# Performance work log

Hardware: AMD Instinct MI355X
Metric: run time of the kernel (lower is better)

## Reference

```python
import jax, jax.numpy as jnp
import numpy as np

H = 4          # attention heads
C = 64         # per-head channels (hidden_size)
NEG_SLOPE = 0.2  # PyG GATConv default negative_slope


def _gat_layer(x, W, a_src, a_dst, b, src, dst):
    """PyG-style GATConv (concat=True) on one graph. x: [N, F]."""
    N = x.shape[0]
    h = (x @ W).reshape(N, H, C)                      # [N, H, C]
    s_src = jnp.sum(h * a_src, axis=-1)               # [N, H]
    s_dst = jnp.sum(h * a_dst, axis=-1)               # [N, H]
    e = jax.nn.leaky_relu(s_src[src] + s_dst[dst], NEG_SLOPE)   # [E, H]
    # softmax over incoming edges of each destination node
    m = jax.ops.segment_max(e, dst, num_segments=N)   # [N, H]
    m = jnp.where(jnp.isfinite(m), m, 0.0)
    ex = jnp.exp(e - m[dst])
    denom = jax.ops.segment_sum(ex, dst, num_segments=N)
    alpha = ex / denom[dst]                           # [E, H]
    out = jax.ops.segment_sum(h[src] * alpha[:, :, None], dst, num_segments=N)
    return out.reshape(N, H * C) + b                  # [N, H*C]


def setup_inputs() -> dict:
    key = jax.random.key(0)
    ks = jax.random.split(key, 12)
    B, N, F = 2, 20000, 128
    E = 320000
    HC = H * C  # 256
    x = jax.random.normal(ks[0], (B, N, F), dtype=jnp.float32)
    edge_index = jax.random.randint(ks[1], (2, E), 0, N, dtype=jnp.int64)
    def glorot(k, shape):
        fan = shape[0] + shape[-1]
        return jax.random.normal(k, shape, dtype=jnp.float32) * np.sqrt(2.0 / fan)
    return {
        "x": x,
        "edge_index": edge_index,
        "W1": glorot(ks[2], (F, HC)),
        "a_src1": glorot(ks[3], (H, C)),
        "a_dst1": glorot(ks[4], (H, C)),
        "b1": jnp.zeros((HC,), jnp.float32),
        "W2": glorot(ks[5], (HC, HC)),
        "a_src2": glorot(ks[6], (H, C)),
        "a_dst2": glorot(ks[7], (H, C)),
        "b2": jnp.zeros((HC,), jnp.float32),
        "Wf": glorot(ks[8], (HC, C)),
        "bf": jnp.zeros((C,), jnp.float32),
    }


def reference(x, edge_index, W1, a_src1, a_dst1, b1, W2, a_src2, a_dst2, b2, Wf, bf):
    B, N, _ = x.shape
    sl = jnp.arange(N, dtype=edge_index.dtype)        # self loops (PyG default)
    src = jnp.concatenate([edge_index[0], sl])
    dst = jnp.concatenate([edge_index[1], sl])
    h = jax.vmap(lambda xi: _gat_layer(xi, W1, a_src1, a_dst1, b1, src, dst))(x)
    h = jax.nn.elu(h)
    h = jax.vmap(lambda xi: _gat_layer(xi, W2, a_src2, a_dst2, b2, src, dst))(h)
    return h @ Wf + bf                                 # [B, N, hidden]
```

## Files before the change

kernel.cpp:

```cpp
#include <hip/hip_runtime.h>
#include <math.h>

#define NN 20000
#define NE 320000
#define ETOT (NE + NN)
#define NH 4
#define CH 64
#define HC 256
#define FIN 128
#define NEG_SLOPE 0.2f
#define CAP 64
#define EST 68
#define AGG_TPB 128

typedef unsigned short ushort_t;
typedef unsigned int uint_t;
typedef _Float16 half8 __attribute__((ext_vector_type(8)));
typedef float f32x4 __attribute__((ext_vector_type(4)));

__device__ __forceinline__ ushort_t f2h_bits(float f) {
    union { _Float16 h; ushort_t u; } c; c.h = (_Float16)f;
    return c.u;
}


__global__ void k_zero_i32(int* __restrict__ p, int n) {
    int i = blockIdx.x * blockDim.x + threadIdx.x;
    if (i < n) p[i] = 0;
}

__global__ void k_hist(const int* __restrict__ ei, int* __restrict__ counts) {
    int e = blockIdx.x * blockDim.x + threadIdx.x;
    if (e >= ETOT) return;
    int d = (e < NE) ? ei[NE + e] : (e - NE);
    atomicAdd(&counts[d], 1);
}

__global__ void k_scan(const int* __restrict__ counts, int* __restrict__ rowptr,
                       int* __restrict__ cursor) {
    __shared__ int part[1024];
    int tid = threadIdx.x;
    const int n = NN;
    int chunk = (n + 1023) / 1024;
    int b = tid * chunk;
    int e = min(b + chunk, n);
    int s = 0;
    for (int i = b; i < e; ++i) s += counts[i];
    part[tid] = s;
    __syncthreads();
    for (int off = 1; off < 1024; off <<= 1) {
        int v = (tid >= off) ? part[tid - off] : 0;
        __syncthreads();
        part[tid] += v;
        __syncthreads();
    }
    int ex = (tid > 0) ? part[tid - 1] : 0;
    for (int i = b; i < e; ++i) { rowptr[i] = ex; cursor[i] = ex; ex += counts[i]; }
    if (tid == 1023) rowptr[n] = part[1023];
}

__global__ void k_scatter(const int* __restrict__ ei, int* __restrict__ cursor,
                          int* __restrict__ col) {
    int e = blockIdx.x * blockDim.x + threadIdx.x;
    if (e >= ETOT) return;
    int s, d;
    if (e < NE) { s = ei[e]; d = ei[NE + e]; }
    else        { s = e - NE; d = s; }
    int pos = atomicAdd(&cursor[d], 1);
    col[pos] = s;
}


#define SN1 (FIN * HC)
#define SN2 (SN1 + HC * HC)
#define SN3 (SN2 + HC * CH)
#define SN4 (SN3 + (2 * NN * FIN) / 4)

__global__ void k_setup(const float* __restrict__ x, const float* __restrict__ W1,
                        const float* __restrict__ W2, const float* __restrict__ Wf,
                        ushort_t* __restrict__ Xh, ushort_t* __restrict__ Wt1,
                        ushort_t* __restrict__ Wt2, ushort_t* __restrict__ Wtf) {
    int i = blockIdx.x * blockDim.x + threadIdx.x;
    if (i < SN1) {
        int n = i / FIN, k = i - n * FIN;
        Wt1[i] = f2h_bits(W1[(size_t)k * HC + n]);
    } else if (i < SN2) {
        int j = i - SN1;
        int n = j / HC, k = j - n * HC;
        Wt2[j] = f2h_bits(W2[(size_t)k * HC + n]);
    } else if (i < SN3) {
        int j = i - SN2;
        int n = j / HC, k = j - n * HC;
        Wtf[j] = f2h_bits(Wf[(size_t)k * CH + n]);
    } else if (i < SN4) {
        int j = (i - SN3) * 4;
        float4 v = *reinterpret_cast<const float4*>(&x[j]);
        ushort4 u;
        u.x = f2h_bits(v.x); u.y = f2h_bits(v.y); u.z = f2h_bits(v.z); u.w = f2h_bits(v.w);
        *reinterpret_cast<ushort4*>(&Xh[j]) = u;
    }
}


__global__ __launch_bounds__(256) void k_gemm128(const ushort_t* __restrict__ A,
                                                 const ushort_t* __restrict__ Bt,
                                                 ushort_t* __restrict__ Ch,
                                                 const float* __restrict__ a_src,
                                                 const float* __restrict__ a_dst,
                                                 float* __restrict__ ssrc,
                                                 float* __restrict__ sdst,
                                                 int M, int K, int NC) {
    __shared__ ushort_t As[128 * 40];
    __shared__ ushort_t Bs[128 * 40];
    int tid = threadIdx.x;
    int wave = tid >> 6, lane = tid & 63;
    int wr = wave >> 1, wc = wave & 1;
    int row0 = blockIdx.x * 128, col0 = blockIdx.y * 128;

    f32x4 acc[4][4];
#pragma unroll
    for (int i = 0; i < 4; ++i)
#pragma unroll
        for (int j = 0; j < 4; ++j) acc[i][j] = (f32x4){0.f, 0.f, 0.f, 0.f};

    int srow = tid >> 2;
    int sk8 = (tid & 3) * 8;
    int l15 = lane & 15, lk = (lane >> 4) * 8;

    int ra0 = min(row0 + srow, M - 1);
    int ra1 = min(row0 + 64 + srow, M - 1);

    for (int k0 = 0; k0 < K; k0 += 32) {
        uint4 a0 = *reinterpret_cast<const uint4*>(&A[(size_t)ra0 * K + k0 + sk8]);
        uint4 a1 = *reinterpret_cast<const uint4*>(&A[(size_t)ra1 * K + k0 + sk8]);
        uint4 b0 = *reinterpret_cast<const uint4*>(&Bt[(size_t)(col0 + srow) * K + k0 + sk8]);
        uint4 b1 = *reinterpret_cast<const uint4*>(&Bt[(size_t)(col0 + 64 + srow) * K + k0 + sk8]);
        __syncthreads();
        *reinterpret_cast<uint4*>(&As[srow * 40 + sk8]) = a0;
        *reinterpret_cast<uint4*>(&As[(64 + srow) * 40 + sk8]) = a1;
        *reinterpret_cast<uint4*>(&Bs[srow * 40 + sk8]) = b0;
        *reinterpret_cast<uint4*>(&Bs[(64 + srow) * 40 + sk8]) = b1;
        __syncthreads();

        half8 af[4], bf_[4];
#pragma unroll
        for (int m = 0; m < 4; ++m)
            af[m] = *reinterpret_cast<const half8*>(&As[(wr * 64 + m * 16 + l15) * 40 + lk]);
#pragma unroll
        for (int nf = 0; nf < 4; ++nf)
            bf_[nf] = *reinterpret_cast<const half8*>(&Bs[(wc * 64 + nf * 16 + l15) * 40 + lk]);
#pragma unroll
        for (int m = 0; m < 4; ++m)
#pragma unroll
            for (int nf = 0; nf < 4; ++nf)
                acc[m][nf] = __builtin_amdgcn_mfma_f32_16x16x32_f16(af[m], bf_[nf], acc[m][nf], 0, 0, 0);
    }

#pragma unroll
    for (int m = 0; m < 4; ++m)
#pragma unroll
        for (int nf = 0; nf < 4; ++nf) {
            int colc = col0 + wc * 64 + nf * 16 + l15;
#pragma unroll
            for (int j = 0; j < 4; ++j) {
                int row = row0 + wr * 64 + m * 16 + (lane >> 4) * 4 + j;
                if (row < M) Ch[(size_t)row * NC + colc] = f2h_bits(acc[m][nf][j]);
            }
        }

    if (ssrc) {
        int head = (col0 >> 6) + wc;
        float as4[4], ad4[4];
#pragma unroll
        for (int nf = 0; nf < 4; ++nf) {
            as4[nf] = a_src[head * 64 + nf * 16 + l15];
            ad4[nf] = a_dst[head * 64 + nf * 16 + l15];
        }
#pragma unroll
        for (int m = 0; m < 4; ++m)
#pragma unroll
            for (int j = 0; j < 4; ++j) {
                float ps = acc[m][0][j] * as4[0] + acc[m][1][j] * as4[1]
                         + acc[m][2][j] * as4[2] + acc[m][3][j] * as4[3];
                float pd = acc[m][0][j] * ad4[0] + acc[m][1][j] * ad4[1]
                         + acc[m][2][j] * ad4[2] + acc[m][3][j] * ad4[3];
#pragma unroll
                for (int off = 1; off < 16; off <<= 1) {
                    ps += __shfl_xor(ps, off);
                    pd += __shfl_xor(pd, off);
                }
                int row = row0 + wr * 64 + m * 16 + (lane >> 4) * 4 + j;
                if (l15 == 0 && row < M) {
                    ssrc[(size_t)row * NH + head] = ps;
                    sdst[(size_t)row * NH + head] = pd;
                }
            }
    }
}


__global__ __launch_bounds__(256) void k_gemm_mfma(const ushort_t* __restrict__ A,
                                                   const ushort_t* __restrict__ Bt,
                                                   float* __restrict__ Cf,
                                                   const float* __restrict__ bias,
                                                   int M, int K, int NC) {
    __shared__ ushort_t As[64][40];
    __shared__ ushort_t Bs[64][40];
    int tid = threadIdx.x;
    int wave = tid >> 6, lane = tid & 63;
    int wr = wave >> 1, wc = wave & 1;
    int row0 = blockIdx.x * 64, col0 = blockIdx.y * 64;

    f32x4 acc[2][2];
#pragma unroll
    for (int i = 0; i < 2; ++i)
#pragma unroll
        for (int j = 0; j < 2; ++j) acc[i][j] = (f32x4){0.f, 0.f, 0.f, 0.f};

    int sr = tid >> 2;
    int sk = (tid & 3) * 8;
    int l15 = lane & 15, lk = (lane >> 4) * 8;

    for (int k0 = 0; k0 < K; k0 += 32) {
        uint4 av = make_uint4(0, 0, 0, 0);
        int rowg = row0 + sr;
        if (rowg < M) av = *reinterpret_cast<const uint4*>(&A[(size_t)rowg * K + k0 + sk]);
        uint4 bv = *reinterpret_cast<const uint4*>(&Bt[(size_t)(col0 + sr) * K + k0 + sk]);
        __syncthreads();
        *reinterpret_cast<uint4*>(&As[sr][sk]) = av;
        *reinterpret_cast<uint4*>(&Bs[sr][sk]) = bv;
        __syncthreads();

        half8 a0 = *reinterpret_cast<const half8*>(&As[wr * 32 + l15][lk]);
        half8 a1 = *reinterpret_cast<const half8*>(&As[wr * 32 + 16 + l15][lk]);
        half8 b0 = *reinterpret_cast<const half8*>(&Bs[wc * 32 + l15][lk]);
        half8 b1 = *reinterpret_cast<const half8*>(&Bs[wc * 32 + 16 + l15][lk]);
        acc[0][0] = __builtin_amdgcn_mfma_f32_16x16x32_f16(a0, b0, acc[0][0], 0, 0, 0);
        acc[0][1] = __builtin_amdgcn_mfma_f32_16x16x32_f16(a0, b1, acc[0][1], 0, 0, 0);
        acc[1][0] = __builtin_amdgcn_mfma_f32_16x16x32_f16(a1, b0, acc[1][0], 0, 0, 0);
        acc[1][1] = __builtin_amdgcn_mfma_f32_16x16x32_f16(a1, b1, acc[1][1], 0, 0, 0);
    }

#pragma unroll
    for (int fr = 0; fr < 2; ++fr)
#pragma unroll
        for (int fc = 0; fc < 2; ++fc) {
            int colc = col0 + wc * 32 + fc * 16 + l15;
#pragma unroll
            for (int j = 0; j < 4; ++j) {
                int row = row0 + wr * 32 + fr * 16 + (lane >> 4) * 4 + j;
                if (row < M) Cf[(size_t)row * NC + colc] = acc[fr][fc][j] + bias[colc];
            }
        }
}


__global__ __launch_bounds__(AGG_TPB) void k_agg(const ushort_t* __restrict__ hb,
                                                 const float* __restrict__ ssrc,
                                                 const float* __restrict__ sdst,
                                                 const int* __restrict__ rowptr,
                                                 const int* __restrict__ col,
                                                 const float* __restrict__ bias,
                                                 ushort_t* __restrict__ outh,
                                                 int do_elu) {
    __shared__ int cols_lds[AGG_TPB / 64][CAP];
    __shared__ float e_lds[AGG_TPB / 64][4 * EST];
    int wave = threadIdx.x >> 6, lane = threadIdx.x & 63;
    int gw = blockIdx.x * (AGG_TPB / 64) + wave;
    int b = (gw >= NN) ? 1 : 0;
    int n = gw - b * NN;
    int* colw = cols_lds[wave];
    float* ew = e_lds[wave];
    int start = rowptr[n];
    int deg = rowptr[n + 1] - start;
    int es = lane >> 5;
    int cg = lane & 31;
    int hd = cg >> 3;

    const ushort_t* hbase = hb + (size_t)b * NN * HC;
    const float* ssrcb = ssrc + (size_t)b * NN * NH;

    float sd[4];
    {
        float4 s0 = *reinterpret_cast<const float4*>(&sdst[((size_t)b * NN + n) * NH]);
        sd[0] = s0.x; sd[1] = s0.y; sd[2] = s0.z; sd[3] = s0.w;
    }

    float pd[4], acc[8];
#pragma unroll
    for (int c = 0; c < 4; ++c) pd[c] = 0.f;
#pragma unroll
    for (int j = 0; j < 8; ++j) acc[j] = 0.f;

    const int cg8 = cg * 8;

    for (int c0 = 0; c0 < deg; c0 += CAP) {
        int cnt = min(CAP, deg - c0);
        int cnt4 = (cnt + 3) & ~3;

        for (int i = lane; i < cnt4; i += 64) {
            if (i < cnt) {
                int s = col[start + c0 + i];
                colw[i] = s * HC;
                float4 p = *reinterpret_cast<const float4*>(&ssrcb[(size_t)s * NH]);
                float e[4];
                e[0] = p.x + sd[0]; e[1] = p.y + sd[1]; e[2] = p.z + sd[2]; e[3] = p.w + sd[3];
#pragma unroll
                for (int c = 0; c < 4; ++c) {
                    e[c] = fmaxf(e[c], NEG_SLOPE * e[c]);
                    float w = __expf(e[c]);
                    ew[c * EST + i] = w;
                    pd[c] += w;
                }
            } else {
                colw[i] = 0;
#pragma unroll
                for (int c = 0; c < 4; ++c) ew[c * EST + i] = 0.f;
            }
        }

        for (int i = 0; i < cnt4; i += 4) {
            int i0 = i + es, i1 = i + 2 + es;
            int o0 = colw[i0], o1 = colw[i1];
            float w0 = ew[hd * EST + i0], w1 = ew[hd * EST + i1];
            half8 v0 = *reinterpret_cast<const half8*>(hbase + o0 + cg8);
            half8 v1 = *reinterpret_cast<const half8*>(hbase + o1 + cg8);
#pragma unroll
            for (int j = 0; j < 8; ++j) acc[j] = fmaf((float)v0[j], w0, acc[j]);
#pragma unroll
            for (int j = 0; j < 8; ++j) acc[j] = fmaf((float)v1[j], w1, acc[j]);
        }
    }

#pragma unroll
    for (int off = 32; off > 0; off >>= 1)
#pragma unroll
        for (int c = 0; c < 4; ++c) pd[c] += __shfl_xor(pd[c], off);

#pragma unroll
    for (int j = 0; j < 8; ++j) acc[j] += __shfl_xor(acc[j], 32);

    if (es == 0) {
        float inv = 1.0f / pd[hd];
        float4 b0 = *reinterpret_cast<const float4*>(&bias[cg8]);
        float4 b1 = *reinterpret_cast<const float4*>(&bias[cg8 + 4]);
        float bv[8] = {b0.x, b0.y, b0.z, b0.w, b1.x, b1.y, b1.z, b1.w};
        ushort_t o[8];
#pragma unroll
        for (int j = 0; j < 8; ++j) {
            float r = acc[j] * inv + bv[j];
            if (do_elu && r < 0.f) r = expm1f(r);
            o[j] = f2h_bits(r);
        }
        *reinterpret_cast<uint4*>(&outh[((size_t)b * NN + n) * HC + cg8]) =
            *reinterpret_cast<uint4*>(&o[0]);
    }
}


extern "C" void kernel_launch(void* const* d_in, const int* in_sizes, int n_in,
                              void* d_out, int out_size, void* d_ws, size_t ws_size,
                              hipStream_t stream) {
    const float* x      = (const float*)d_in[0];
    const int*   ei     = (const int*)d_in[1];
    const float* W1     = (const float*)d_in[2];
    const float* a_src1 = (const float*)d_in[3];
    const float* a_dst1 = (const float*)d_in[4];
    const float* b1     = (const float*)d_in[5];
    const float* W2     = (const float*)d_in[6];
    const float* a_src2 = (const float*)d_in[7];
    const float* a_dst2 = (const float*)d_in[8];
    const float* b2     = (const float*)d_in[9];
    const float* Wf     = (const float*)d_in[10];
    const float* bf     = (const float*)d_in[11];
    float* out = (float*)d_out;

    const int M2 = 2 * NN;
    float* ws = (float*)d_ws;
    float* Ssrc = ws;
    float* Sdst = Ssrc + (size_t)M2 * NH;
    ushort_t* Hb16 = (ushort_t*)(Sdst + (size_t)M2 * NH);
    ushort_t* Ob16 = Hb16 + (size_t)M2 * HC;
    ushort_t* Xb16 = Ob16 + (size_t)M2 * HC;
    ushort_t* Wt1  = Xb16 + (size_t)M2 * FIN;
    ushort_t* Wt2  = Wt1 + (size_t)HC * FIN;
    ushort_t* Wtf  = Wt2 + (size_t)HC * HC;
    int* counts = (int*)(Wtf + (size_t)CH * HC);
    int* rowptr = counts + NN;
    int* cursor = rowptr + (NN + 1);
    int* colidx = cursor + NN;

    k_zero_i32<<<(NN + 255) / 256, 256, 0, stream>>>(counts, NN);
    k_hist<<<(ETOT + 255) / 256, 256, 0, stream>>>(ei, counts);
    k_scan<<<1, 1024, 0, stream>>>(counts, rowptr, cursor);
    k_scatter<<<(ETOT + 255) / 256, 256, 0, stream>>>(ei, cursor, colidx);

    k_setup<<<(SN4 + 255) / 256, 256, 0, stream>>>(x, W1, W2, Wf, Xb16, Wt1, Wt2, Wtf);

    const int gM128 = (M2 + 127) / 128;
    const int gAgg = M2 / (AGG_TPB / 64);
    k_gemm128<<<dim3(gM128, HC / 128), 256, 0, stream>>>(Xb16, Wt1, Hb16, a_src1, a_dst1,
                                                         Ssrc, Sdst, M2, FIN, HC);
    k_agg<<<gAgg, AGG_TPB, 0, stream>>>(Hb16, Ssrc, Sdst, rowptr, colidx, b1, Ob16, 1);
    k_gemm128<<<dim3(gM128, HC / 128), 256, 0, stream>>>(Ob16, Wt2, Hb16, a_src2, a_dst2,
                                                         Ssrc, Sdst, M2, HC, HC);
    k_agg<<<gAgg, AGG_TPB, 0, stream>>>(Hb16, Ssrc, Sdst, rowptr, colidx, b2, Ob16, 0);
    k_gemm_mfma<<<dim3((M2 + 63) / 64, CH / 64), 256, 0, stream>>>(Ob16, Wtf, out, bf, M2, HC, CH);
}
```

Baseline: 221.5 us.

## Parallelize CSR row-pointer scan and make aggregation a persistent grid-stride kernel

```diff
diff --git a/kernel.cpp b/kernel.cpp
--- a/kernel.cpp
+++ b/kernel.cpp
@@ -11,7 +11,9 @@
 #define NEG_SLOPE 0.2f
 #define CAP 64
 #define EST 68
-#define AGG_TPB 128
+#define SCB 79
+#define AGG_BLOCKS 2048
+#define AGG_SLOTS (AGG_BLOCKS * 4)
 
 typedef unsigned short ushort_t;
 typedef unsigned int uint_t;
@@ -36,27 +38,54 @@
     atomicAdd(&counts[d], 1);
 }
 
-__global__ void k_scan(const int* __restrict__ counts, int* __restrict__ rowptr,
-                       int* __restrict__ cursor) {
-    __shared__ int part[1024];
-    int tid = threadIdx.x;
-    const int n = NN;
-    int chunk = (n + 1023) / 1024;
-    int b = tid * chunk;
-    int e = min(b + chunk, n);
-    int s = 0;
-    for (int i = b; i < e; ++i) s += counts[i];
-    part[tid] = s;
+__global__ void k_scan_part(const int* __restrict__ counts, int* __restrict__ bsum) {
+    __shared__ int red[256];
+    int t = threadIdx.x;
+    int i = blockIdx.x * 256 + t;
+    red[t] = (i < NN) ? counts[i] : 0;
     __syncthreads();
-    for (int off = 1; off < 1024; off <<= 1) {
-        int v = (tid >= off) ? part[tid - off] : 0;
-        __syncthreads();
-        part[tid] += v;
-        __syncthreads();
-    }
-    int ex = (tid > 0) ? part[tid - 1] : 0;
-    for (int i = b; i < e; ++i) { rowptr[i] = ex; cursor[i] = ex; ex += counts[i]; }
-    if (tid == 1023) rowptr[n] = part[1023];
+#pragma unroll
+    for (int off = 128; off > 0; off >>= 1) {
+        if (t < off) red[t] += red[t + off];
+        __syncthreads();
+    }
+    if (t == 0) bsum[blockIdx.x] = red[0];
+}
+
+__global__ void k_scan_top(const int* __restrict__ bsum, int* __restrict__ bpre) {
+    __shared__ int s[128];
+    int t = threadIdx.x;
+    int own = (t < SCB) ? bsum[t] : 0;
+    s[t] = own;
+    __syncthreads();
+#pragma unroll
+    for (int off = 1; off < 128; off <<= 1) {
+        int v = (t >= off) ? s[t - off] : 0;
+        __syncthreads();
+        s[t] += v;
+        __syncthreads();
+    }
+    if (t < SCB) bpre[t] = s[t] - own;
+}
+
+__global__ void k_scan_apply(const int* __restrict__ counts, const int* __restrict__ bpre,
+                             int* __restrict__ rowptr, int* __restrict__ cursor) {
+    __shared__ int s[256];
+    int t = threadIdx.x;
+    int i = blockIdx.x * 256 + t;
+    int c = (i < NN) ? counts[i] : 0;
+    s[t] = c;
+    __syncthreads();
+#pragma unroll
+    for (int off = 1; off < 256; off <<= 1) {
+        int v = (t >= off) ? s[t - off] : 0;
+        __syncthreads();
+        s[t] += v;
+        __syncthreads();
+    }
+    int ex = s[t] - c + bpre[blockIdx.x];
+    if (i < NN) { rowptr[i] = ex; cursor[i] = ex; }
+    if (i == NN - 1) rowptr[NN] = ex + c;
 }
 
 __global__ void k_scatter(const int* __restrict__ ei, int* __restrict__ cursor,
@@ -255,105 +284,108 @@
 }
 
 
-__global__ __launch_bounds__(AGG_TPB) void k_agg(const ushort_t* __restrict__ hb,
-                                                 const float* __restrict__ ssrc,
-                                                 const float* __restrict__ sdst,
-                                                 const int* __restrict__ rowptr,
-                                                 const int* __restrict__ col,
-                                                 const float* __restrict__ bias,
-                                                 ushort_t* __restrict__ outh,
-                                                 int do_elu) {
-    __shared__ int cols_lds[AGG_TPB / 64][CAP];
-    __shared__ float e_lds[AGG_TPB / 64][4 * EST];
+__global__ __launch_bounds__(256) void k_agg(const ushort_t* __restrict__ hb,
+                                             const float* __restrict__ ssrc,
+                                             const float* __restrict__ sdst,
+                                             const int* __restrict__ rowptr,
+                                             const int* __restrict__ col,
+                                             const float* __restrict__ bias,
+                                             ushort_t* __restrict__ outh,
+                                             int do_elu) {
+    __shared__ int cols_lds[4][CAP];
+    __shared__ float e_lds[4][4 * EST];
     int wave = threadIdx.x >> 6, lane = threadIdx.x & 63;
-    int gw = blockIdx.x * (AGG_TPB / 64) + wave;
-    int b = (gw >= NN) ? 1 : 0;
-    int n = gw - b * NN;
+    int slot = blockIdx.x * 4 + wave;
     int* colw = cols_lds[wave];
     float* ew = e_lds[wave];
-    int start = rowptr[n];
-    int deg = rowptr[n + 1] - start;
     int es = lane >> 5;
     int cg = lane & 31;
     int hd = cg >> 3;
-
-    const ushort_t* hbase = hb + (size_t)b * NN * HC;
-    const float* ssrcb = ssrc + (size_t)b * NN * NH;
-
-    float sd[4];
-    {
-        float4 s0 = *reinterpret_cast<const float4*>(&sdst[((size_t)b * NN + n) * NH]);
-        sd[0] = s0.x; sd[1] = s0.y; sd[2] = s0.z; sd[3] = s0.w;
-    }
-
-    float pd[4], acc[8];
-#pragma unroll
-    for (int c = 0; c < 4; ++c) pd[c] = 0.f;
-#pragma unroll
-    for (int j = 0; j < 8; ++j) acc[j] = 0.f;
-
     const int cg8 = cg * 8;
 
-    for (int c0 = 0; c0 < deg; c0 += CAP) {
-        int cnt = min(CAP, deg - c0);
-        int cnt4 = (cnt + 3) & ~3;
-
-        for (int i = lane; i < cnt4; i += 64) {
-            if (i < cnt) {
-                int s = col[start + c0 + i];
-                colw[i] = s * HC;
-                float4 p = *reinterpret_cast<const float4*>(&ssrcb[(size_t)s * NH]);
-                float e[4];
-                e[0] = p.x + sd[0]; e[1] = p.y + sd[1]; e[2] = p.z + sd[2]; e[3] = p.w + sd[3];
-#pragma unroll
-                for (int c = 0; c < 4; ++c) {
-                    e[c] = fmaxf(e[c], NEG_SLOPE * e[c]);
-                    float w = __expf(e[c]);
-                    ew[c * EST + i] = w;
-                    pd[c] += w;
+    for (int gw = slot; gw < 2 * NN; gw += AGG_SLOTS) {
+        int b = (gw >= NN) ? 1 : 0;
+        int n = gw - b * NN;
+        int start = rowptr[n];
+        int deg = rowptr[n + 1] - start;
+
+        const ushort_t* hbase = hb + (size_t)b * NN * HC;
+        const float* ssrcb = ssrc + (size_t)b * NN * NH;
+
+        float sd[4];
+        {
+            float4 s0 = *reinterpret_cast<const float4*>(&sdst[((size_t)b * NN + n) * NH]);
+            sd[0] = s0.x; sd[1] = s0.y; sd[2] = s0.z; sd[3] = s0.w;
+        }
+
+        float pd[4], acc[8];
+#pragma unroll
+        for (int c = 0; c < 4; ++c) pd[c] = 0.f;
+#pragma unroll
+        for (int j = 0; j < 8; ++j) acc[j] = 0.f;
+
+        for (int c0 = 0; c0 < deg; c0 += CAP) {
+            int cnt = min(CAP, deg - c0);
+            int cnt4 = (cnt + 3) & ~3;
+
+            for (int i = lane; i < cnt4; i += 64) {
+                if (i < cnt) {
+                    int s = col[start + c0 + i];
+                    colw[i] = s * HC;
+                    float4 p = *reinterpret_cast<const float4*>(&ssrcb[(size_t)s * NH]);
+                    float e[4];
+                    e[0] = p.x + sd[0]; e[1] = p.y + sd[1];
+                    e[2] = p.z + sd[2]; e[3] = p.w + sd[3];
+#pragma unroll
+                    for (int c = 0; c < 4; ++c) {
+                        e[c] = fmaxf(e[c], NEG_SLOPE * e[c]);
+                        float w = __expf(e[c]);
+                        ew[c * EST + i] = w;
+                        pd[c] += w;
+                    }
+                } else {
+                    colw[i] = 0;
+#pragma unroll
+                    for (int c = 0; c < 4; ++c) ew[c * EST + i] = 0.f;
                 }
-            } else {
-                colw[i] = 0;
-#pragma unroll
-                for (int c = 0; c < 4; ++c) ew[c * EST + i] = 0.f;
-            }
-        }
-
-        for (int i = 0; i < cnt4; i += 4) {
-            int i0 = i + es, i1 = i + 2 + es;
-            int o0 = colw[i0], o1 = colw[i1];
-            float w0 = ew[hd * EST + i0], w1 = ew[hd * EST + i1];
-            half8 v0 = *reinterpret_cast<const half8*>(hbase + o0 + cg8);
-            half8 v1 = *reinterpret_cast<const half8*>(hbase + o1 + cg8);
-#pragma unroll
-            for (int j = 0; j < 8; ++j) acc[j] = fmaf((float)v0[j], w0, acc[j]);
-#pragma unroll
-            for (int j = 0; j < 8; ++j) acc[j] = fmaf((float)v1[j], w1, acc[j]);
-        }
-    }
-
-#pragma unroll
-    for (int off = 32; off > 0; off >>= 1)
-#pragma unroll
-        for (int c = 0; c < 4; ++c) pd[c] += __shfl_xor(pd[c], off);
-
-#pragma unroll
-    for (int j = 0; j < 8; ++j) acc[j] += __shfl_xor(acc[j], 32);
-
-    if (es == 0) {
-        float inv = 1.0f / pd[hd];
-        float4 b0 = *reinterpret_cast<const float4*>(&bias[cg8]);
-        float4 b1 = *reinterpret_cast<const float4*>(&bias[cg8 + 4]);
-        float bv[8] = {b0.x, b0.y, b0.z, b0.w, b1.x, b1.y, b1.z, b1.w};
-        ushort_t o[8];
-#pragma unroll
-        for (int j = 0; j < 8; ++j) {
-            float r = acc[j] * inv + bv[j];
-            if (do_elu && r < 0.f) r = expm1f(r);
-            o[j] = f2h_bits(r);
-        }
-        *reinterpret_cast<uint4*>(&outh[((size_t)b * NN + n) * HC + cg8]) =
-            *reinterpret_cast<uint4*>(&o[0]);
+            }
+
+            for (int i = 0; i < cnt4; i += 4) {
+                int i0 = i + es, i1 = i + 2 + es;
+                int o0 = colw[i0], o1 = colw[i1];
+                float w0 = ew[hd * EST + i0], w1 = ew[hd * EST + i1];
+                half8 v0 = *reinterpret_cast<const half8*>(hbase + o0 + cg8);
+                half8 v1 = *reinterpret_cast<const half8*>(hbase + o1 + cg8);
+#pragma unroll
+                for (int j = 0; j < 8; ++j) acc[j] = fmaf((float)v0[j], w0, acc[j]);
+#pragma unroll
+                for (int j = 0; j < 8; ++j) acc[j] = fmaf((float)v1[j], w1, acc[j]);
+            }
+        }
+
+#pragma unroll
+        for (int off = 32; off > 0; off >>= 1)
+#pragma unroll
+            for (int c = 0; c < 4; ++c) pd[c] += __shfl_xor(pd[c], off);
+
+#pragma unroll
+        for (int j = 0; j < 8; ++j) acc[j] += __shfl_xor(acc[j], 32);
+
+        if (es == 0) {
+            float inv = 1.0f / pd[hd];
+            float4 b0 = *reinterpret_cast<const float4*>(&bias[cg8]);
+            float4 b1 = *reinterpret_cast<const float4*>(&bias[cg8 + 4]);
+            float bv[8] = {b0.x, b0.y, b0.z, b0.w, b1.x, b1.y, b1.z, b1.w};
+            ushort_t o[8];
+#pragma unroll
+            for (int j = 0; j < 8; ++j) {
+                float r = acc[j] * inv + bv[j];
+                if (do_elu && r < 0.f) r = expm1f(r);
+                o[j] = f2h_bits(r);
+            }
+            *reinterpret_cast<uint4*>(&outh[((size_t)b * NN + n) * HC + cg8]) =
+                *reinterpret_cast<uint4*>(&o[0]);
+        }
     }
 }
 
@@ -389,21 +421,24 @@
     int* rowptr = counts + NN;
     int* cursor = rowptr + (NN + 1);
     int* colidx = cursor + NN;
+    int* bsum   = colidx + ETOT;
+    int* bpre   = bsum + SCB;
 
     k_zero_i32<<<(NN + 255) / 256, 256, 0, stream>>>(counts, NN);
     k_hist<<<(ETOT + 255) / 256, 256, 0, stream>>>(ei, counts);
-    k_scan<<<1, 1024, 0, stream>>>(counts, rowptr, cursor);
+    k_scan_part<<<SCB, 256, 0, stream>>>(counts, bsum);
+    k_scan_top<<<1, 128, 0, stream>>>(bsum, bpre);
+    k_scan_apply<<<SCB, 256, 0, stream>>>(counts, bpre, rowptr, cursor);
     k_scatter<<<(ETOT + 255) / 256, 256, 0, stream>>>(ei, cursor, colidx);
 
     k_setup<<<(SN4 + 255) / 256, 256, 0, stream>>>(x, W1, W2, Wf, Xb16, Wt1, Wt2, Wtf);
 
     const int gM128 = (M2 + 127) / 128;
-    const int gAgg = M2 / (AGG_TPB / 64);
     k_gemm128<<<dim3(gM128, HC / 128), 256, 0, stream>>>(Xb16, Wt1, Hb16, a_src1, a_dst1,
                                                          Ssrc, Sdst, M2, FIN, HC);
-    k_agg<<<gAgg, AGG_TPB, 0, stream>>>(Hb16, Ssrc, Sdst, rowptr, colidx, b1, Ob16, 1);
+    k_agg<<<AGG_BLOCKS, 256, 0, stream>>>(Hb16, Ssrc, Sdst, rowptr, colidx, b1, Ob16, 1);
     k_gemm128<<<dim3(gM128, HC / 128), 256, 0, stream>>>(Ob16, Wt2, Hb16, a_src2, a_dst2,
                                                          Ssrc, Sdst, M2, HC, HC);
-    k_agg<<<gAgg, AGG_TPB, 0, stream>>>(Hb16, Ssrc, Sdst, rowptr, colidx, b2, Ob16, 0);
+    k_agg<<<AGG_BLOCKS, 256, 0, stream>>>(Hb16, Ssrc, Sdst, rowptr, colidx, b2, Ob16, 0);
     k_gemm_mfma<<<dim3((M2 + 63) / 64, CH / 64), 256, 0, stream>>>(Ob16, Wtf, out, bf, M2, HC, CH);
 }
```

Result: faster. 211.9 us (-4.3%).
